# Performance work log

Measured on AMD Instinct MI355X. Metric: run time of the kernel, lower is better.

The kernel has to match this reference:

```python
import jax, jax.numpy as jnp
import numpy as np

N = 20000          # cells (graph nodes)
E = 320000         # edges (avg degree 16)
IN, MID, OUT = 2, 128, 3
HEADS = (4, 4, 1)
CONCAT = (False, False, True)
BN_EPS = 1e-5


def setup_inputs() -> dict:
    key = jax.random.key(0)
    ks = jax.random.split(key, 40)
    f32 = jnp.float32
    inp = {
        "x": jax.random.normal(ks[0], (N, IN), f32),
        "edge_index": jax.random.randint(ks[1], (2, E), 0, N, jnp.int32),
        "gene_index": 0,
    }
    in_dims = (IN, MID, MID)
    out_dims = (MID, MID, OUT)
    i = 2
    for L in range(3):
        H, C = HEADS[L], out_dims[L]
        inp[f"W{L}"] = jax.random.normal(ks[i], (H * C, in_dims[L]), f32) * 0.1; i += 1
        inp[f"as{L}"] = jax.random.normal(ks[i], (H, C), f32) * 0.1; i += 1
        inp[f"ad{L}"] = jax.random.normal(ks[i], (H, C), f32) * 0.1; i += 1
        bdim = H * C if CONCAT[L] else C
        inp[f"b{L}"] = jax.random.normal(ks[i], (bdim,), f32) * 0.1; i += 1
    for L in range(2):
        inp[f"bn_g{L}"] = 1.0 + jax.random.normal(ks[i], (MID,), f32) * 0.1; i += 1
        inp[f"bn_b{L}"] = jax.random.normal(ks[i], (MID,), f32) * 0.1; i += 1
        inp[f"bn_m{L}"] = jax.random.normal(ks[i], (MID,), f32) * 0.1; i += 1
        inp[f"bn_v{L}"] = jax.random.uniform(ks[i], (MID,), f32, minval=0.5, maxval=1.5); i += 1
    inp["k"] = jax.random.normal(ks[i], (1,), f32); i += 1
    inp["d"] = jax.random.normal(ks[i], (1,), f32) * 0.1; i += 1
    inp["t0"] = jax.random.uniform(ks[i], (1,), f32) * 0.2; i += 1
    inp["u0"] = jax.random.uniform(ks[i], (1,), f32); i += 1
    inp["t"] = jax.random.uniform(ks[i], (N, 1), f32); i += 1
    return inp


def _gat(x, W, a_s, a_d, b, src, dst, heads, concat):
    # PyG GATConv (eval): linear -> per-node head scores -> edge leaky_relu
    # -> segment softmax over dst -> scatter-weighted aggregate -> bias.
    n = x.shape[0]
    h = (x @ W.T).reshape(n, heads, -1)                      # [N,H,C]
    logit = jax.nn.leaky_relu(
        (h * a_s).sum(-1)[src] + (h * a_d).sum(-1)[dst], 0.2)  # [E,H]
    m = jax.ops.segment_max(logit, dst, num_segments=n)
    p = jnp.exp(logit - m[dst])
    alpha = p / (jax.ops.segment_sum(p, dst, num_segments=n)[dst] + 1e-16)
    out = jax.ops.segment_sum(h[src] * alpha[:, :, None], dst, num_segments=n)
    out = out.reshape(n, -1) if concat else out.mean(axis=1)
    return out + b


def _forward(x, edge_index, gene_index,
             W0, as0, ad0, b0, W1, as1, ad1, b1, W2, as2, ad2, b2,
             bn_g0, bn_b0, bn_m0, bn_v0, bn_g1, bn_b1, bn_m1, bn_v1,
             k, d, t0, u0, t):
    n = x.shape[0]
    loop = jnp.arange(n, dtype=edge_index.dtype)             # add_self_loops=True
    src = jnp.concatenate([edge_index[0], loop])
    dst = jnp.concatenate([edge_index[1], loop])
    convs = ((W0, as0, ad0, b0), (W1, as1, ad1, b1), (W2, as2, ad2, b2))
    bns = ((bn_g0, bn_b0, bn_m0, bn_v0), (bn_g1, bn_b1, bn_m1, bn_v1))
    for L in range(3):
        W, a_s, a_d, b = convs[L]
        x = jax.nn.elu(_gat(x, W, a_s, a_d, b, src, dst, HEADS[L], CONCAT[L]))
        if L != 2:
            g_, b_, m_, v_ = bns[L]
            x = (x - m_) * jax.lax.rsqrt(v_ + BN_EPS) * g_ + b_   # BN eval
            # dropout is a no-op in eval mode
    a_r = x[:, 0]
    gam = x[:, 1]
    bet = x[:, 2]
    g = gene_index
    tt = t[:, g]
    S = jax.nn.sigmoid(k[g] * (tt - t0[g] - d[g]))
    eb = jnp.exp(-bet * tt)
    eg = jnp.exp(-gam * tt)
    ebs = jnp.exp(-bet * (tt - t0[g]))
    egs = jnp.exp(-gam * (tt - t0[g]))
    ab = a_r / bet
    ag = a_r / gam
    tilde_u = ab * (1 - eb) * (1 - S) + ab * S + (u0[g] * ebs - ab) * S
    tilde_s = (ag * (1 - eg) + a_r / (gam - bet) * (eg - eb)) * (1 - S) \
              + ag * S + bet * u0[g] / (gam - bet) * (egs - ebs) * S
    return tilde_u, tilde_s


def reference(x, edge_index, gene_index,
              W0, as0, ad0, b0, W1, as1, ad1, b1, W2, as2, ad2, b2,
              bn_g0, bn_b0, bn_m0, bn_v0, bn_g1, bn_b1, bn_m1, bn_v1,
              k, d, t0, u0, t):
    return _forward(x, edge_index, gene_index,
                    W0, as0, ad0, b0, W1, as1, ad1, b1, W2, as2, ad2, b2,
                    bn_g0, bn_b0, bn_m0, bn_v0, bn_g1, bn_b1, bn_m1, bn_v1,
                    k, d, t0, u0, t)
```

## Files before the change

### kernel.cpp

```cpp
#include <hip/hip_runtime.h>
#include <hip/hip_bf16.h>

#define CAP 64

__device__ __forceinline__ float eluf(float x){ return x > 0.f ? x : expm1f(x); }
__device__ __forceinline__ float lrelu(float x){ return x >= 0.f ? x : 0.2f*x; }

__device__ __forceinline__ float ldf(const void* p, size_t i, int f){
  if(f) return ((const float*)p)[i];
  unsigned u = ((const unsigned short*)p)[i];
  return __uint_as_float(u << 16);
}

__device__ __forceinline__ unsigned pk2(float a, float b){
  __hip_bfloat16 ba = __float2bfloat16(a), bb = __float2bfloat16(b);
  unsigned short ua = *(unsigned short*)&ba, ub = *(unsigned short*)&bb;
  return (unsigned)ua | ((unsigned)ub << 16);
}
__device__ __forceinline__ float lo16(unsigned u){ return __uint_as_float(u << 16); }
__device__ __forceinline__ float hi16(unsigned u){ return __uint_as_float(u & 0xffff0000u); }

__device__ __forceinline__ float4 shfl4(float4 v, int m){
  return make_float4(__shfl_xor(v.x,m), __shfl_xor(v.y,m), __shfl_xor(v.z,m), __shfl_xor(v.w,m));
}
__device__ __forceinline__ float4 max4(float4 a, float4 b){
  return make_float4(fmaxf(a.x,b.x), fmaxf(a.y,b.y), fmaxf(a.z,b.z), fmaxf(a.w,b.w));
}
__device__ __forceinline__ float4 add4(float4 a, float4 b){
  return make_float4(a.x+b.x, a.y+b.y, a.z+b.z, a.w+b.w);
}

__global__ void zero_detect(const unsigned short* __restrict__ w1raw, int* __restrict__ flag,
                            int* __restrict__ cursor, int N){
  int i = blockIdx.x*256 + threadIdx.x;
  if(i < N) cursor[i] = 0;
  if(blockIdx.x == 0){
    __shared__ int cnt;
    if(threadIdx.x == 0) cnt = 0;
    __syncthreads();
    int c = 0;
    for(int k = threadIdx.x; k < 2048; k += 256){
      unsigned int u = w1raw[2*k];
      float v = __uint_as_float(u << 16);
      if(fabsf(v) > 100.f) c++;
    }
    atomicAdd(&cnt, c);
    __syncthreads();
    if(threadIdx.x == 0) *flag = (cnt > 10) ? 1 : 0;
  }
}

#define NSEG 21
struct CvtDesc {
  const void* src[NSEG];
  float*      dst[NSEG];
  int         n[NSEG];
};
struct POff { int o[26]; };

__global__ void prep(CvtDesc cd, POff po, const int* __restrict__ flag,
    const void* __restrict__ W0r, const void* __restrict__ as0r, const void* __restrict__ ad0r,
    const void* __restrict__ W1r, const void* __restrict__ as1r, const void* __restrict__ ad1r,
    float* __restrict__ W1t, float* __restrict__ W1sa, float* __restrict__ W1da,
    float* __restrict__ W0sa, float* __restrict__ W0da,
    const int* __restrict__ ei, int E, int N,
    int* __restrict__ cursor, int* __restrict__ csr){
  int bid = blockIdx.x, t = threadIdx.x;
  int sec = 0;
  while(sec < 24 && bid >= po.o[sec+1]) sec++;
  int lb = bid - po.o[sec];
  int f = *flag;
  if(sec < NSEG){
    int i = lb*256 + t;
    if(i < cd.n[sec]) cd.dst[sec][i] = ldf(cd.src[sec], i, f);
  } else if(sec == NSEG){
    int id = lb*256 + t;
    if(id < 512*128){ int ch = id >> 7, k = id & 127; W1t[k*512 + ch] = ldf(W1r, id, f); }
  } else if(sec == NSEG+1){
    int e = lb*256 + t, Et = E + N;
    if(e < Et){
      int s, d;
      if(e < E){ s = ei[e]; d = ei[E + e]; } else { s = d = e - E; }
      int pos = atomicAdd(&cursor[d], 1);
      if(pos < CAP) csr[(size_t)d*CAP + pos] = s;
    }
  } else if(sec == NSEG+2){
    int idx = lb*256 + t;
    if(idx < 1024){
      int k = idx & 127, h = (idx >> 7) & 3, w = idx >> 9;
      const void* A = w ? ad1r : as1r;
      float s = 0.f;
      for(int c = 0; c < 128; c++)
        s += ldf(W1r, (size_t)(h*128+c)*128 + k, f) * ldf(A, h*128+c, f);
      (w ? W1da : W1sa)[k*4 + h] = s;
    }
  } else {
    int idx = lb*256 + t;
    if(idx < 16){
      int col = idx & 1, h = (idx >> 1) & 3, w = idx >> 3;
      const void* A = w ? ad0r : as0r;
      float s = 0.f;
      for(int c = 0; c < 128; c++)
        s += ldf(W0r, (size_t)(h*128+c)*2 + col, f) * ldf(A, h*128+c, f);
      (w ? W0da : W0sa)[h*2 + col] = s;
    }
  }
}

__global__ __launch_bounds__(256) void gather0(
    const int* __restrict__ cursor, const int* __restrict__ csr,
    const float* __restrict__ xf,
    const float* __restrict__ W0f,
    const float* __restrict__ W0sa, const float* __restrict__ W0da,
    const float* __restrict__ b0,
    const float* __restrict__ bn_g, const float* __restrict__ bn_b,
    const float* __restrict__ bn_m, const float* __restrict__ bn_v,
    float* __restrict__ xout){
  int t = threadIdx.x, wv = t >> 6, lane = t & 63;
  int n = blockIdx.x*4 + wv;
  int cnt = min(cursor[n], CAP);
  float2 xn = ((const float2*)xf)[n];
  float4 sd4;
  sd4.x = xn.x*W0da[0] + xn.y*W0da[1];
  sd4.y = xn.x*W0da[2] + xn.y*W0da[3];
  sd4.z = xn.x*W0da[4] + xn.y*W0da[5];
  sd4.w = xn.x*W0da[6] + xn.y*W0da[7];
  float2 xs = make_float2(0.f, 0.f);
  float4 lg = make_float4(-3.0e38f, -3.0e38f, -3.0e38f, -3.0e38f);
  if(lane < cnt){
    int src = csr[(size_t)n*CAP + lane];
    xs = ((const float2*)xf)[src];
    lg.x = lrelu(xs.x*W0sa[0] + xs.y*W0sa[1] + sd4.x);
    lg.y = lrelu(xs.x*W0sa[2] + xs.y*W0sa[3] + sd4.y);
    lg.z = lrelu(xs.x*W0sa[4] + xs.y*W0sa[5] + sd4.z);
    lg.w = lrelu(xs.x*W0sa[6] + xs.y*W0sa[7] + sd4.w);
  }
  float4 mx = lg;
  #pragma unroll
  for(int o = 1; o < 64; o <<= 1) mx = max4(mx, shfl4(mx, o));
  float4 p = make_float4(0.f,0.f,0.f,0.f);
  if(lane < cnt){
    p.x = expf(lg.x - mx.x); p.y = expf(lg.y - mx.y);
    p.z = expf(lg.z - mx.z); p.w = expf(lg.w - mx.w);
  }
  float4 dn = p;
  #pragma unroll
  for(int o = 1; o < 64; o <<= 1) dn = add4(dn, shfl4(dn, o));
  float4 ax = make_float4(0.f,0.f,0.f,0.f);
  float4 ay = make_float4(0.f,0.f,0.f,0.f);
  if(lane < cnt){
    float4 al;
    al.x = p.x/(dn.x + 1e-16f); al.y = p.y/(dn.y + 1e-16f);
    al.z = p.z/(dn.z + 1e-16f); al.w = p.w/(dn.w + 1e-16f);
    ax = make_float4(al.x*xs.x, al.y*xs.x, al.z*xs.x, al.w*xs.x);
    ay = make_float4(al.x*xs.y, al.y*xs.y, al.z*xs.y, al.w*xs.y);
  }
  #pragma unroll
  for(int o = 1; o < 64; o <<= 1){ ax = add4(ax, shfl4(ax, o)); ay = add4(ay, shfl4(ay, o)); }
  float o2[2];
  #pragma unroll
  for(int i = 0; i < 2; i++){
    int c = 2*lane + i;
    float acc = W0f[(c      )*2]*ax.x + W0f[(c      )*2+1]*ay.x
              + W0f[(128 + c)*2]*ax.y + W0f[(128 + c)*2+1]*ay.y
              + W0f[(256 + c)*2]*ax.z + W0f[(256 + c)*2+1]*ay.z
              + W0f[(384 + c)*2]*ax.w + W0f[(384 + c)*2+1]*ay.w;
    float v = 0.25f*acc + b0[c];
    v = eluf(v);
    float sc = bn_g[c] * rsqrtf(bn_v[c] + 1e-5f);
    o2[i] = (v - bn_m[c])*sc + bn_b[c];
  }
  ((float2*)(xout + (size_t)n*128))[lane] = make_float2(o2[0], o2[1]);
}

__global__ __launch_bounds__(256) void linear1_tiled(const float* __restrict__ x1,
    const float* __restrict__ W1t, const float* __restrict__ W1sa, const float* __restrict__ W1da,
    unsigned* __restrict__ hb, float* __restrict__ ssrc, float* __restrict__ sdst){
  __shared__ float xs[16][128];
  int t = threadIdx.x;
  int base = blockIdx.x*16;
  for(int i = t; i < 2048; i += 256) xs[i>>7][i&127] = x1[(size_t)base*128 + i];
  __syncthreads();
  float2 acc[16];
  #pragma unroll
  for(int n = 0; n < 16; n++) acc[n] = make_float2(0.f, 0.f);
  const float2* Wp = (const float2*)W1t;
  for(int k4 = 0; k4 < 128; k4 += 4){
    float2 w0 = Wp[(k4+0)*256 + t];
    float2 w1 = Wp[(k4+1)*256 + t];
    float2 w2 = Wp[(k4+2)*256 + t];
    float2 w3 = Wp[(k4+3)*256 + t];
    #pragma unroll
    for(int n = 0; n < 16; n++){
      float4 xv = *(const float4*)&xs[n][k4];
      acc[n].x += xv.x*w0.x; acc[n].y += xv.x*w0.y;
      acc[n].x += xv.y*w1.x; acc[n].y += xv.y*w1.y;
      acc[n].x += xv.z*w2.x; acc[n].y += xv.z*w2.y;
      acc[n].x += xv.w*w3.x; acc[n].y += xv.w*w3.y;
    }
  }
  #pragma unroll
  for(int n = 0; n < 16; n++)
    hb[(size_t)(base+n)*256 + t] = pk2(acc[n].x, acc[n].y);
  if(t < 128){
    int nl = t >> 3, o = t & 7, h = o & 3, w = o >> 2;
    const float* Wa = w ? W1da : W1sa;
    float s = 0.f;
    for(int k4 = 0; k4 < 128; k4 += 4){
      float4 xv = *(const float4*)&xs[nl][k4];
      s += xv.x*Wa[(k4+0)*4+h] + xv.y*Wa[(k4+1)*4+h]
         + xv.z*Wa[(k4+2)*4+h] + xv.w*Wa[(k4+3)*4+h];
    }
    (w ? sdst : ssrc)[(size_t)(base+nl)*4 + h] = s;
  }
}

__global__ __launch_bounds__(128) void gather_bn(
    const int* __restrict__ cursor, const int* __restrict__ csr,
    const float* __restrict__ s_src, const float* __restrict__ s_dst,
    const unsigned* __restrict__ hb,
    const float* __restrict__ bias,
    const float* __restrict__ bn_g, const float* __restrict__ bn_b,
    const float* __restrict__ bn_m, const float* __restrict__ bn_v,
    float* __restrict__ xout){
  __shared__ int   srcs[CAP];
  __shared__ float lp[CAP*4];
  __shared__ float mi[8];
  __shared__ float4 red[32];
  int n = blockIdx.x, t = threadIdx.x;
  int cnt = min(cursor[n], CAP);
  const int* row = csr + (size_t)n*CAP;
  for(int i = t; i < cnt; i += 128) srcs[i] = row[i];
  __syncthreads();
  for(int i = t; i < cnt*4; i += 128){
    int j = i >> 2, h = i & 3;
    lp[i] = lrelu(s_src[srcs[j]*4 + h] + s_dst[n*4 + h]);
  }
  __syncthreads();
  if(t < 4){
    float mm = -3.0e38f;
    for(int j = 0; j < cnt; j++) mm = fmaxf(mm, lp[j*4 + t]);
    float s = 0.f;
    for(int j = 0; j < cnt; j++) s += expf(lp[j*4 + t] - mm);
    mi[t] = mm; mi[4 + t] = 1.f/(s + 1e-16f);
  }
  __syncthreads();
  for(int i = t; i < cnt*4; i += 128){
    int h = i & 3;
    lp[i] = expf(lp[i] - mi[h]) * mi[4 + h];
  }
  __syncthreads();
  int h = t >> 5, gq = t & 31;
  const char* hbp = (const char*)hb + h*256 + gq*8;
  float4 acc = make_float4(0.f,0.f,0.f,0.f);
  int j = 0;
  for(; j + 2 <= cnt; j += 2){
    uint2 u0 = *(const uint2*)(hbp + ((size_t)srcs[j]   << 10));
    uint2 u1 = *(const uint2*)(hbp + ((size_t)srcs[j+1] << 10));
    float a0 = lp[j*4 + h], a1 = lp[(j+1)*4 + h];
    acc.x += a0*lo16(u0.x); acc.y += a0*hi16(u0.x);
    acc.z += a0*lo16(u0.y); acc.w += a0*hi16(u0.y);
    acc.x += a1*lo16(u1.x); acc.y += a1*hi16(u1.x);
    acc.z += a1*lo16(u1.y); acc.w += a1*hi16(u1.y);
  }
  if(j < cnt){
    uint2 u0 = *(const uint2*)(hbp + ((size_t)srcs[j] << 10));
    float a0 = lp[j*4 + h];
    acc.x += a0*lo16(u0.x); acc.y += a0*hi16(u0.x);
    acc.z += a0*lo16(u0.y); acc.w += a0*hi16(u0.y);
  }
  acc.x += __shfl_xor(acc.x, 32);
  acc.y += __shfl_xor(acc.y, 32);
  acc.z += __shfl_xor(acc.z, 32);
  acc.w += __shfl_xor(acc.w, 32);
  if(t >= 64 && t < 96) red[t - 64] = acc;
  __syncthreads();
  if(t < 32){
    float4 o = red[t];
    acc.x += o.x; acc.y += o.y; acc.z += o.z; acc.w += o.w;
    float4 bi = ((const float4*)bias)[t];
    float4 gg = ((const float4*)bn_g)[t];
    float4 bb = ((const float4*)bn_b)[t];
    float4 mm = ((const float4*)bn_m)[t];
    float4 vv = ((const float4*)bn_v)[t];
    float4 r;
    r.x = (eluf(0.25f*acc.x + bi.x) - mm.x)*(gg.x*rsqrtf(vv.x + 1e-5f)) + bb.x;
    r.y = (eluf(0.25f*acc.y + bi.y) - mm.y)*(gg.y*rsqrtf(vv.y + 1e-5f)) + bb.y;
    r.z = (eluf(0.25f*acc.z + bi.z) - mm.z)*(gg.z*rsqrtf(vv.z + 1e-5f)) + bb.z;
    r.w = (eluf(0.25f*acc.w + bi.w) - mm.w)*(gg.w*rsqrtf(vv.w + 1e-5f)) + bb.w;
    ((float4*)(xout + (size_t)n*128))[t] = r;
  }
}

__global__ __launch_bounds__(256) void linear2(const float* __restrict__ xin,
    const float* __restrict__ W2f,
    const float* __restrict__ as2f, const float* __restrict__ ad2f,
    float* __restrict__ h2, float* __restrict__ s_src,
    float* __restrict__ s_dst, int N){
  int t = threadIdx.x;
  int n = blockIdx.x*64 + (t >> 2);
  if(n >= N) return;
  int q = t & 3;
  const float4* xp = (const float4*)(xin + (size_t)n*128);
  float c0 = 0.f, c1 = 0.f, c2 = 0.f;
  for(int qq = q; qq < 32; qq += 4){
    float4 xv = xp[qq];
    float4 w0 = ((const float4*)(W2f      ))[qq];
    float4 w1 = ((const float4*)(W2f + 128))[qq];
    float4 w2 = ((const float4*)(W2f + 256))[qq];
    c0 += xv.x*w0.x + xv.y*w0.y + xv.z*w0.z + xv.w*w0.w;
    c1 += xv.x*w1.x + xv.y*w1.y + xv.z*w1.z + xv.w*w1.w;
    c2 += xv.x*w2.x + xv.y*w2.y + xv.z*w2.z + xv.w*w2.w;
  }
  c0 += __shfl_xor(c0, 1); c0 += __shfl_xor(c0, 2);
  c1 += __shfl_xor(c1, 1); c1 += __shfl_xor(c1, 2);
  c2 += __shfl_xor(c2, 1); c2 += __shfl_xor(c2, 2);
  if(q == 0){
    ((float4*)h2)[n] = make_float4(c0, c1, c2, 0.f);
    s_src[n] = c0*as2f[0] + c1*as2f[1] + c2*as2f[2];
    s_dst[n] = c0*ad2f[0] + c1*ad2f[1] + c2*ad2f[2];
  }
}

__global__ __launch_bounds__(256) void gather_ode(const int* __restrict__ cursor,
    const int* __restrict__ csr,
    const float* __restrict__ s_src, const float* __restrict__ s_dst,
    const float* __restrict__ h2, const float* __restrict__ b2f,
    const float* __restrict__ scal,
    const float* __restrict__ tf, float* __restrict__ out, int N){
  int n = (blockIdx.x*256 + threadIdx.x) >> 6;
  if(n >= N) return;
  int lane = threadIdx.x & 63;
  int cnt = min(cursor[n], CAP);
  const int* row = csr + (size_t)n*CAP;
  float sd = s_dst[n];
  int s = 0; float logit = -3.0e38f;
  if(lane < cnt){ s = row[lane]; logit = lrelu(s_src[s] + sd); }
  float m = logit;
  #pragma unroll
  for(int o = 32; o > 0; o >>= 1) m = fmaxf(m, __shfl_xor(m, o));
  float pw = (lane < cnt) ? expf(logit - m) : 0.f;
  float4 hv = (lane < cnt) ? ((const float4*)h2)[s] : make_float4(0,0,0,0);
  float den = pw, a0 = pw*hv.x, a1 = pw*hv.y, a2 = pw*hv.z;
  #pragma unroll
  for(int o = 32; o > 0; o >>= 1){
    den += __shfl_xor(den, o);
    a0  += __shfl_xor(a0, o);
    a1  += __shfl_xor(a1, o);
    a2  += __shfl_xor(a2, o);
  }
  if(lane != 0) return;
  double inv = 1.0/((double)den + 1e-16);
  double A0 = (double)a0*inv + (double)b2f[0];
  double A1 = (double)a1*inv + (double)b2f[1];
  double A2 = (double)a2*inv + (double)b2f[2];
  double ar  = A0 > 0.0 ? A0 : expm1(A0);
  double gam = A1 > 0.0 ? A1 : expm1(A1);
  double bet = A2 > 0.0 ? A2 : expm1(A2);
  double tt = (double)tf[n];
  double k = (double)scal[0], d = (double)scal[1];
  double t0 = (double)scal[2], u0 = (double)scal[3];
  double S = 1.0/(1.0 + exp(-(k*(tt - t0 - d))));
  double eb  = exp(-bet*tt),        eg  = exp(-gam*tt);
  double ebs = exp(-bet*(tt - t0)), egs = exp(-gam*(tt - t0));
  double ab = ar/bet, ag = ar/gam;
  double tu = ab*(1.0 - eb)*(1.0 - S) + ab*S + (u0*ebs - ab)*S;
  double gmb = gam - bet;
  double ts = (ag*(1.0 - eg) + ar/gmb*(eg - eb))*(1.0 - S) + ag*S
            + bet*u0/gmb*(egs - ebs)*S;
  out[n]     = (float)tu;
  out[N + n] = (float)ts;
}

extern "C" void kernel_launch(void* const* d_in, const int* in_sizes, int n_in,
                              void* d_out, int out_size, void* d_ws, size_t ws_size,
                              hipStream_t stream) {
  const int* ei = (const int*)d_in[1];
  int N = in_sizes[0] / 2;
  int E = in_sizes[1] / 2;
  int Et = E + N;

  char* ws = (char*)d_ws;
  size_t off = 0;
  auto alloc = [&](size_t bytes)->void*{
    void* p = ws + off; off += (bytes + 255) & ~(size_t)255; return p;
  };
  int*   flag  = (int*)  alloc(4);
  float* xf    = (float*)alloc((size_t)N*2*4);
  float* W0f   = (float*)alloc(1024*4);
  float* b0f   = (float*)alloc(128*4);
  float* b1f   = (float*)alloc(128*4);
  float* W2f   = (float*)alloc(384*4);
  float* as2f  = (float*)alloc(3*4);
  float* ad2f  = (float*)alloc(3*4);
  float* b2f   = (float*)alloc(3*4);
  float* bnf[8];
  for(int i = 0; i < 8; i++) bnf[i] = (float*)alloc(128*4);
  float* scal  = (float*)alloc(4*4);
  float* tf    = (float*)alloc((size_t)N*4);
  float* W1t   = (float*)alloc(65536*4);
  float* W1sa  = (float*)alloc(512*4);
  float* W1da  = (float*)alloc(512*4);
  float* W0sa  = (float*)alloc(8*4);
  float* W0da  = (float*)alloc(8*4);
  int*   cursor= (int*)  alloc((size_t)N*4);
  int*   csr   = (int*)  alloc((size_t)N*CAP*4);
  unsigned* hb = (unsigned*)alloc((size_t)N*512*2);
  float* x1    = (float*)alloc((size_t)N*128*4);
  float* h2    = (float*)alloc((size_t)N*4*4);
  float* ssrc  = (float*)alloc((size_t)N*4*4);
  float* sdst  = (float*)alloc((size_t)N*4*4);

  zero_detect<<<(N + 255)/256, 256, 0, stream>>>((const unsigned short*)d_in[7], flag, cursor, N);

  CvtDesc cd;
  const int src_idx[NSEG] = {0,3,6,10, 11,12,13,14, 15,16,17,18,19,20,21,22, 23,24,25,26, 27};
  float* dsts[NSEG] = {xf,W0f,b0f,b1f, W2f,as2f,ad2f,b2f,
                       bnf[0],bnf[1],bnf[2],bnf[3],bnf[4],bnf[5],bnf[6],bnf[7],
                       scal+0,scal+1,scal+2,scal+3, tf};
  for(int i = 0; i < NSEG; i++){
    cd.src[i] = d_in[src_idx[i]];
    cd.dst[i] = dsts[i];
    cd.n[i]   = in_sizes[src_idx[i]];
  }
  POff po;
  int acc = 0;
  for(int i = 0; i < NSEG; i++){ po.o[i] = acc; acc += (cd.n[i] + 255)/256; }
  po.o[NSEG] = acc;   acc += 256;
  po.o[NSEG+1] = acc; acc += (Et + 255)/256;
  po.o[NSEG+2] = acc; acc += 4;
  po.o[NSEG+3] = acc; acc += 1;
  po.o[NSEG+4] = acc;
  prep<<<acc, 256, 0, stream>>>(cd, po, flag,
      d_in[3], d_in[4], d_in[5], d_in[7], d_in[8], d_in[9],
      W1t, W1sa, W1da, W0sa, W0da, ei, E, N, cursor, csr);

  gather0<<<N/4, 256, 0, stream>>>(cursor, csr, xf, W0f, W0sa, W0da, b0f,
                                   bnf[0], bnf[1], bnf[2], bnf[3], x1);
  linear1_tiled<<<N/16, 256, 0, stream>>>(x1, W1t, W1sa, W1da, hb, ssrc, sdst);
  gather_bn<<<N, 128, 0, stream>>>(cursor, csr, ssrc, sdst, hb, b1f,
                                   bnf[4], bnf[5], bnf[6], bnf[7], x1);
  linear2<<<(N + 63)/64, 256, 0, stream>>>(x1, W2f, as2f, ad2f, h2, ssrc, sdst, N);
  gather_ode<<<(N*64 + 255)/256, 256, 0, stream>>>(cursor, csr, ssrc, sdst,
                                                   h2, b2f, scal, tf,
                                                   (float*)d_out, N);
}
```

Measured before the change: 298.4 us.

## Aggregate layer-1 inputs before projection and fuse attention scores into gather0

Layer 1 is reordered so that neighbors' 128-dim bf16 inputs are gathered and attention-weighted per head first, and the W1 projection is applied afterwards to the aggregated features. Rows are no longer projected to 512 channels up front and then gathered. The attention source and destination scores are now computed in gather0 from precomputed W1·a vectors, which removes the separate linear1 kernel and its 512-wide bf16 intermediate. The trade is a per-node 512x128 matmul in gather1 over 16-node tiles, read from a re-laid-out W1. Layer-1 inputs are also quantized to bf16 before aggregation, which adds precision risk.

```diff
diff --git a/kernel.cpp b/kernel.cpp
--- a/kernel.cpp
+++ b/kernel.cpp
@@ -61,7 +61,7 @@
 __global__ void prep(CvtDesc cd, POff po, const int* __restrict__ flag,
     const void* __restrict__ W0r, const void* __restrict__ as0r, const void* __restrict__ ad0r,
     const void* __restrict__ W1r, const void* __restrict__ as1r, const void* __restrict__ ad1r,
-    float* __restrict__ W1t, float* __restrict__ W1sa, float* __restrict__ W1da,
+    float* __restrict__ W1g4, float* __restrict__ W1sa, float* __restrict__ W1da,
     float* __restrict__ W0sa, float* __restrict__ W0da,
     const int* __restrict__ ei, int E, int N,
     int* __restrict__ cursor, int* __restrict__ csr){
@@ -75,7 +75,11 @@
     if(i < cd.n[sec]) cd.dst[sec][i] = ldf(cd.src[sec], i, f);
   } else if(sec == NSEG){
     int id = lb*256 + t;
-    if(id < 512*128){ int ch = id >> 7, k = id & 127; W1t[k*512 + ch] = ldf(W1r, id, f); }
+    if(id < 512*128){
+      int m = id >> 7, c = id & 127;
+      int h = m >> 7, k = m & 127;
+      W1g4[(size_t)(m >> 2)*512 + c*4 + (m & 3)] = ldf(W1r, (size_t)(h*128 + c)*128 + k, f);
+    }
   } else if(sec == NSEG+1){
     int e = lb*256 + t, Et = E + N;
     if(e < Et){
@@ -112,10 +116,12 @@
     const float* __restrict__ xf,
     const float* __restrict__ W0f,
     const float* __restrict__ W0sa, const float* __restrict__ W0da,
+    const float* __restrict__ W1sa, const float* __restrict__ W1da,
     const float* __restrict__ b0,
     const float* __restrict__ bn_g, const float* __restrict__ bn_b,
     const float* __restrict__ bn_m, const float* __restrict__ bn_v,
-    float* __restrict__ xout){
+    unsigned* __restrict__ x1b,
+    float* __restrict__ ssrc, float* __restrict__ sdst){
   int t = threadIdx.x, wv = t >> 6, lane = t & 63;
   int n = blockIdx.x*4 + wv;
   int cnt = min(cursor[n], CAP);
@@ -170,125 +176,113 @@
     float sc = bn_g[c] * rsqrtf(bn_v[c] + 1e-5f);
     o2[i] = (v - bn_m[c])*sc + bn_b[c];
   }
-  ((float2*)(xout + (size_t)n*128))[lane] = make_float2(o2[0], o2[1]);
-}
-
-__global__ __launch_bounds__(256) void linear1_tiled(const float* __restrict__ x1,
-    const float* __restrict__ W1t, const float* __restrict__ W1sa, const float* __restrict__ W1da,
-    unsigned* __restrict__ hb, float* __restrict__ ssrc, float* __restrict__ sdst){
-  __shared__ float xs[16][128];
-  int t = threadIdx.x;
-  int base = blockIdx.x*16;
-  for(int i = t; i < 2048; i += 256) xs[i>>7][i&127] = x1[(size_t)base*128 + i];
-  __syncthreads();
-  float2 acc[16];
-  #pragma unroll
-  for(int n = 0; n < 16; n++) acc[n] = make_float2(0.f, 0.f);
-  const float2* Wp = (const float2*)W1t;
-  for(int k4 = 0; k4 < 128; k4 += 4){
-    float2 w0 = Wp[(k4+0)*256 + t];
-    float2 w1 = Wp[(k4+1)*256 + t];
-    float2 w2 = Wp[(k4+2)*256 + t];
-    float2 w3 = Wp[(k4+3)*256 + t];
-    #pragma unroll
-    for(int n = 0; n < 16; n++){
-      float4 xv = *(const float4*)&xs[n][k4];
-      acc[n].x += xv.x*w0.x; acc[n].y += xv.x*w0.y;
-      acc[n].x += xv.y*w1.x; acc[n].y += xv.y*w1.y;
-      acc[n].x += xv.z*w2.x; acc[n].y += xv.z*w2.y;
-      acc[n].x += xv.w*w3.x; acc[n].y += xv.w*w3.y;
-    }
-  }
-  #pragma unroll
-  for(int n = 0; n < 16; n++)
-    hb[(size_t)(base+n)*256 + t] = pk2(acc[n].x, acc[n].y);
-  if(t < 128){
-    int nl = t >> 3, o = t & 7, h = o & 3, w = o >> 2;
-    const float* Wa = w ? W1da : W1sa;
-    float s = 0.f;
-    for(int k4 = 0; k4 < 128; k4 += 4){
-      float4 xv = *(const float4*)&xs[nl][k4];
-      s += xv.x*Wa[(k4+0)*4+h] + xv.y*Wa[(k4+1)*4+h]
-         + xv.z*Wa[(k4+2)*4+h] + xv.w*Wa[(k4+3)*4+h];
-    }
-    (w ? sdst : ssrc)[(size_t)(base+nl)*4 + h] = s;
-  }
-}
-
-__global__ __launch_bounds__(128) void gather_bn(
+  x1b[(size_t)n*64 + lane] = pk2(o2[0], o2[1]);
+  float4 ws0 = ((const float4*)W1sa)[2*lane];
+  float4 ws1 = ((const float4*)W1sa)[2*lane + 1];
+  float4 wd0 = ((const float4*)W1da)[2*lane];
+  float4 wd1 = ((const float4*)W1da)[2*lane + 1];
+  float4 ps, pd;
+  ps.x = o2[0]*ws0.x + o2[1]*ws1.x; ps.y = o2[0]*ws0.y + o2[1]*ws1.y;
+  ps.z = o2[0]*ws0.z + o2[1]*ws1.z; ps.w = o2[0]*ws0.w + o2[1]*ws1.w;
+  pd.x = o2[0]*wd0.x + o2[1]*wd1.x; pd.y = o2[0]*wd0.y + o2[1]*wd1.y;
+  pd.z = o2[0]*wd0.z + o2[1]*wd1.z; pd.w = o2[0]*wd0.w + o2[1]*wd1.w;
+  #pragma unroll
+  for(int o = 1; o < 64; o <<= 1){ ps = add4(ps, shfl4(ps, o)); pd = add4(pd, shfl4(pd, o)); }
+  if(lane == 0){
+    ((float4*)ssrc)[n] = ps;
+    ((float4*)sdst)[n] = pd;
+  }
+}
+
+__global__ __launch_bounds__(256) void gather1(
     const int* __restrict__ cursor, const int* __restrict__ csr,
     const float* __restrict__ s_src, const float* __restrict__ s_dst,
-    const unsigned* __restrict__ hb,
-    const float* __restrict__ bias,
+    const unsigned* __restrict__ x1b,
+    const float* __restrict__ W1g4,
+    const float* __restrict__ b1,
     const float* __restrict__ bn_g, const float* __restrict__ bn_b,
     const float* __restrict__ bn_m, const float* __restrict__ bn_v,
-    float* __restrict__ xout){
-  __shared__ int   srcs[CAP];
-  __shared__ float lp[CAP*4];
-  __shared__ float mi[8];
-  __shared__ float4 red[32];
-  int n = blockIdx.x, t = threadIdx.x;
-  int cnt = min(cursor[n], CAP);
-  const int* row = csr + (size_t)n*CAP;
-  for(int i = t; i < cnt; i += 128) srcs[i] = row[i];
+    float* __restrict__ x2){
+  __shared__ float lal[4][CAP*4];
+  __shared__ int   lsr[4][CAP];
+  __shared__ float sS[16][512];
+  int t = threadIdx.x, wv = t >> 6, lane = t & 63;
+  int base = blockIdx.x*16;
+  for(int nl = 0; nl < 4; nl++){
+    int n = base + wv*4 + nl;
+    int cnt = min(cursor[n], CAP);
+    float4 sd4 = ((const float4*)s_dst)[n];
+    float4 lg = make_float4(-3.0e38f, -3.0e38f, -3.0e38f, -3.0e38f);
+    if(lane < cnt){
+      int src = csr[(size_t)n*CAP + lane];
+      lsr[wv][lane] = src;
+      float4 ss4 = ((const float4*)s_src)[src];
+      lg.x = lrelu(ss4.x + sd4.x); lg.y = lrelu(ss4.y + sd4.y);
+      lg.z = lrelu(ss4.z + sd4.z); lg.w = lrelu(ss4.w + sd4.w);
+    }
+    float4 mx = lg;
+    #pragma unroll
+    for(int o = 1; o < 64; o <<= 1) mx = max4(mx, shfl4(mx, o));
+    float4 p = make_float4(0.f,0.f,0.f,0.f);
+    if(lane < cnt){
+      p.x = expf(lg.x - mx.x); p.y = expf(lg.y - mx.y);
+      p.z = expf(lg.z - mx.z); p.w = expf(lg.w - mx.w);
+    }
+    float4 dn = p;
+    #pragma unroll
+    for(int o = 1; o < 64; o <<= 1) dn = add4(dn, shfl4(dn, o));
+    if(lane < cnt){
+      float4 al;
+      al.x = p.x/(dn.x + 1e-16f); al.y = p.y/(dn.y + 1e-16f);
+      al.z = p.z/(dn.z + 1e-16f); al.w = p.w/(dn.w + 1e-16f);
+      ((float4*)lal[wv])[lane] = al;
+    }
+    float a0=0,a1=0,a2=0,a3=0,a4=0,a5=0,a6=0,a7=0;
+    int j = 0;
+    for(; j + 2 <= cnt; j += 2){
+      unsigned u0 = x1b[(size_t)lsr[wv][j]  *64 + lane];
+      unsigned u1 = x1b[(size_t)lsr[wv][j+1]*64 + lane];
+      float4 al0 = ((const float4*)lal[wv])[j];
+      float4 al1 = ((const float4*)lal[wv])[j+1];
+      float c00 = lo16(u0), c01 = hi16(u0);
+      float c10 = lo16(u1), c11 = hi16(u1);
+      a0 += al0.x*c00; a1 += al0.x*c01; a2 += al0.y*c00; a3 += al0.y*c01;
+      a4 += al0.z*c00; a5 += al0.z*c01; a6 += al0.w*c00; a7 += al0.w*c01;
+      a0 += al1.x*c10; a1 += al1.x*c11; a2 += al1.y*c10; a3 += al1.y*c11;
+      a4 += al1.z*c10; a5 += al1.z*c11; a6 += al1.w*c10; a7 += al1.w*c11;
+    }
+    if(j < cnt){
+      unsigned u0 = x1b[(size_t)lsr[wv][j]*64 + lane];
+      float4 al0 = ((const float4*)lal[wv])[j];
+      float c00 = lo16(u0), c01 = hi16(u0);
+      a0 += al0.x*c00; a1 += al0.x*c01; a2 += al0.y*c00; a3 += al0.y*c01;
+      a4 += al0.z*c00; a5 += al0.z*c01; a6 += al0.w*c00; a7 += al0.w*c01;
+    }
+    int nn = wv*4 + nl;
+    *(float2*)&sS[nn][0*128 + 2*lane] = make_float2(a0, a1);
+    *(float2*)&sS[nn][1*128 + 2*lane] = make_float2(a2, a3);
+    *(float2*)&sS[nn][2*128 + 2*lane] = make_float2(a4, a5);
+    *(float2*)&sS[nn][3*128 + 2*lane] = make_float2(a6, a7);
+  }
   __syncthreads();
-  for(int i = t; i < cnt*4; i += 128){
-    int j = i >> 2, h = i & 3;
-    lp[i] = lrelu(s_src[srcs[j]*4 + h] + s_dst[n*4 + h]);
-  }
-  __syncthreads();
-  if(t < 4){
-    float mm = -3.0e38f;
-    for(int j = 0; j < cnt; j++) mm = fmaxf(mm, lp[j*4 + t]);
-    float s = 0.f;
-    for(int j = 0; j < cnt; j++) s += expf(lp[j*4 + t] - mm);
-    mi[t] = mm; mi[4 + t] = 1.f/(s + 1e-16f);
-  }
-  __syncthreads();
-  for(int i = t; i < cnt*4; i += 128){
-    int h = i & 3;
-    lp[i] = expf(lp[i] - mi[h]) * mi[4 + h];
-  }
-  __syncthreads();
-  int h = t >> 5, gq = t & 31;
-  const char* hbp = (const char*)hb + h*256 + gq*8;
-  float4 acc = make_float4(0.f,0.f,0.f,0.f);
-  int j = 0;
-  for(; j + 2 <= cnt; j += 2){
-    uint2 u0 = *(const uint2*)(hbp + ((size_t)srcs[j]   << 10));
-    uint2 u1 = *(const uint2*)(hbp + ((size_t)srcs[j+1] << 10));
-    float a0 = lp[j*4 + h], a1 = lp[(j+1)*4 + h];
-    acc.x += a0*lo16(u0.x); acc.y += a0*hi16(u0.x);
-    acc.z += a0*lo16(u0.y); acc.w += a0*hi16(u0.y);
-    acc.x += a1*lo16(u1.x); acc.y += a1*hi16(u1.x);
-    acc.z += a1*lo16(u1.y); acc.w += a1*hi16(u1.y);
-  }
-  if(j < cnt){
-    uint2 u0 = *(const uint2*)(hbp + ((size_t)srcs[j] << 10));
-    float a0 = lp[j*4 + h];
-    acc.x += a0*lo16(u0.x); acc.y += a0*hi16(u0.x);
-    acc.z += a0*lo16(u0.y); acc.w += a0*hi16(u0.y);
-  }
-  acc.x += __shfl_xor(acc.x, 32);
-  acc.y += __shfl_xor(acc.y, 32);
-  acc.z += __shfl_xor(acc.z, 32);
-  acc.w += __shfl_xor(acc.w, 32);
-  if(t >= 64 && t < 96) red[t - 64] = acc;
-  __syncthreads();
-  if(t < 32){
-    float4 o = red[t];
-    acc.x += o.x; acc.y += o.y; acc.z += o.z; acc.w += o.w;
-    float4 bi = ((const float4*)bias)[t];
-    float4 gg = ((const float4*)bn_g)[t];
-    float4 bb = ((const float4*)bn_b)[t];
-    float4 mm = ((const float4*)bn_m)[t];
-    float4 vv = ((const float4*)bn_v)[t];
-    float4 r;
-    r.x = (eluf(0.25f*acc.x + bi.x) - mm.x)*(gg.x*rsqrtf(vv.x + 1e-5f)) + bb.x;
-    r.y = (eluf(0.25f*acc.y + bi.y) - mm.y)*(gg.y*rsqrtf(vv.y + 1e-5f)) + bb.y;
-    r.z = (eluf(0.25f*acc.z + bi.z) - mm.z)*(gg.z*rsqrtf(vv.z + 1e-5f)) + bb.z;
-    r.w = (eluf(0.25f*acc.w + bi.w) - mm.w)*(gg.w*rsqrtf(vv.w + 1e-5f)) + bb.w;
-    ((float4*)(xout + (size_t)n*128))[t] = r;
+  int c = t & 127, half = t >> 7;
+  float acc[8] = {0,0,0,0,0,0,0,0};
+  const float4* Wp = (const float4*)W1g4;
+  for(int m4 = 0; m4 < 128; m4++){
+    float4 w4 = Wp[m4*128 + c];
+    #pragma unroll
+    for(int i = 0; i < 8; i++){
+      float4 sv = *(const float4*)&sS[half*8 + i][m4*4];
+      acc[i] += w4.x*sv.x + w4.y*sv.y + w4.z*sv.z + w4.w*sv.w;
+    }
+  }
+  float bc = b1[c];
+  float sc = bn_g[c] * rsqrtf(bn_v[c] + 1e-5f);
+  float mc = bn_m[c], bb = bn_b[c];
+  #pragma unroll
+  for(int i = 0; i < 8; i++){
+    float v = eluf(0.25f*acc[i] + bc);
+    x2[(size_t)(base + half*8 + i)*128 + c] = (v - mc)*sc + bb;
   }
 }
 
@@ -398,15 +392,15 @@
   for(int i = 0; i < 8; i++) bnf[i] = (float*)alloc(128*4);
   float* scal  = (float*)alloc(4*4);
   float* tf    = (float*)alloc((size_t)N*4);
-  float* W1t   = (float*)alloc(65536*4);
+  float* W1g4  = (float*)alloc(65536*4);
   float* W1sa  = (float*)alloc(512*4);
   float* W1da  = (float*)alloc(512*4);
   float* W0sa  = (float*)alloc(8*4);
   float* W0da  = (float*)alloc(8*4);
   int*   cursor= (int*)  alloc((size_t)N*4);
   int*   csr   = (int*)  alloc((size_t)N*CAP*4);
-  unsigned* hb = (unsigned*)alloc((size_t)N*512*2);
-  float* x1    = (float*)alloc((size_t)N*128*4);
+  unsigned* x1b= (unsigned*)alloc((size_t)N*64*4);
+  float* x2    = (float*)alloc((size_t)N*128*4);
   float* h2    = (float*)alloc((size_t)N*4*4);
   float* ssrc  = (float*)alloc((size_t)N*4*4);
   float* sdst  = (float*)alloc((size_t)N*4*4);
@@ -433,14 +427,13 @@
   po.o[NSEG+4] = acc;
   prep<<<acc, 256, 0, stream>>>(cd, po, flag,
       d_in[3], d_in[4], d_in[5], d_in[7], d_in[8], d_in[9],
-      W1t, W1sa, W1da, W0sa, W0da, ei, E, N, cursor, csr);
-
-  gather0<<<N/4, 256, 0, stream>>>(cursor, csr, xf, W0f, W0sa, W0da, b0f,
-                                   bnf[0], bnf[1], bnf[2], bnf[3], x1);
-  linear1_tiled<<<N/16, 256, 0, stream>>>(x1, W1t, W1sa, W1da, hb, ssrc, sdst);
-  gather_bn<<<N, 128, 0, stream>>>(cursor, csr, ssrc, sdst, hb, b1f,
-                                   bnf[4], bnf[5], bnf[6], bnf[7], x1);
-  linear2<<<(N + 63)/64, 256, 0, stream>>>(x1, W2f, as2f, ad2f, h2, ssrc, sdst, N);
+      W1g4, W1sa, W1da, W0sa, W0da, ei, E, N, cursor, csr);
+
+  gather0<<<N/4, 256, 0, stream>>>(cursor, csr, xf, W0f, W0sa, W0da, W1sa, W1da, b0f,
+                                   bnf[0], bnf[1], bnf[2], bnf[3], x1b, ssrc, sdst);
+  gather1<<<N/16, 256, 0, stream>>>(cursor, csr, ssrc, sdst, x1b, W1g4, b1f,
+                                    bnf[4], bnf[5], bnf[6], bnf[7], x2);
+  linear2<<<(N + 63)/64, 256, 0, stream>>>(x2, W2f, as2f, ad2f, h2, ssrc, sdst, N);
   gather_ode<<<(N*64 + 255)/256, 256, 0, stream>>>(cursor, csr, ssrc, sdst,
                                                    h2, b2f, scal, tf,
                                                    (float*)d_out, N);
```

After: 297.2 us. Within noise of the previous version (-0.4%).
